# Optimization experiments

Measured on AMD Instinct MI355X. Metric: run time of the kernel, lower is better.

## Reference

```python
import jax, jax.numpy as jnp
import numpy as np

HEADS = 8
DIM_HEAD = 64

def setup_inputs() -> dict:
    key = jax.random.key(0)
    ks = jax.random.split(key, 5)
    B, N, D = 2, 4096, 512  # query_dim = inner_dim = 512
    s = 0.02
    return {
        "x": jax.random.normal(ks[0], (B, N, D), dtype=jnp.float32),
        "Wq": jax.random.normal(ks[1], (D, D), dtype=jnp.float32) * s,
        "Wk": jax.random.normal(ks[2], (D, D), dtype=jnp.float32) * s,
        "Wv": jax.random.normal(ks[3], (D, D), dtype=jnp.float32) * s,
        "Wo": jax.random.normal(ks[4], (D, D), dtype=jnp.float32) * s,
        "bo": jnp.zeros((D,), dtype=jnp.float32),
    }

def reference(x, Wq, Wk, Wv, Wo, bo):
    B, N, D = x.shape
    h, dh = HEADS, DIM_HEAD
    scale = dh ** (-0.5)
    # self-attention: context = x
    q = x @ Wq  # [B, N, h*dh]
    k = x @ Wk
    v = x @ Wv
    # b n (h d) -> b h n d
    q = q.reshape(B, N, h, dh).transpose(0, 2, 1, 3)
    k = k.reshape(B, N, h, dh).transpose(0, 2, 1, 3)
    v = v.reshape(B, N, h, dh).transpose(0, 2, 1, 3)
    sim = jnp.einsum('bhid,bhjd->bhij', q, k) * scale  # full [B,h,N,N] matrix
    attn = jax.nn.softmax(sim, axis=-1)
    out = jnp.einsum('bhij,bhjd->bhid', attn, v)
    out = out.transpose(0, 2, 1, 3).reshape(B, N, h * dh)
    return out @ Wo + bo
```

## Files before the change

kernel.cpp:

```cpp
#include <hip/hip_runtime.h>
#include <hip/hip_bf16.h>
#include <stddef.h>
#include <stdint.h>

typedef __bf16 bf16_t;
typedef bf16_t bf16x8 __attribute__((ext_vector_type(8)));
typedef bf16_t bf16x4 __attribute__((ext_vector_type(4)));
typedef bf16_t bf16x2 __attribute__((ext_vector_type(2)));
typedef float floatx4 __attribute__((ext_vector_type(4)));
typedef float floatx16 __attribute__((ext_vector_type(16)));
typedef int   intx4  __attribute__((ext_vector_type(4)));

#define SEQ    4096
#define DMODEL 512
#define NH     8
#define BATCH  2
#define QSCALE 0.18033688011112042f

__device__ __forceinline__ void ld_lds16(const void* g, void* l) {
  __builtin_amdgcn_global_load_lds(
      (const __attribute__((address_space(1))) unsigned int*)g,
      (__attribute__((address_space(3))) unsigned int*)l, 16, 0, 0);
}

__global__ __launch_bounds__(256) void prep_k(
    const float* __restrict__ x,
    const float* __restrict__ W0, const float* __restrict__ W1,
    const float* __restrict__ W2, const float* __restrict__ W3,
    bf16_t* __restrict__ Wt, bf16_t* __restrict__ xb)
{
  if (blockIdx.z == 4) {
    const floatx4* xf = (const floatx4*)x;
    bf16x4* xo = (bf16x4*)xb;
    int base = (blockIdx.y * 16 + blockIdx.x) * 4096 + threadIdx.x;
    #pragma unroll
    for (int i = 0; i < 16; i++) {
      floatx4 v = xf[base + i * 256];
      xo[base + i * 256] = bf16x4{(bf16_t)v.x, (bf16_t)v.y, (bf16_t)v.z, (bf16_t)v.w};
    }
    return;
  }
  __shared__ float Ws[32][33];
  const float* W = (blockIdx.z == 0) ? W0 : (blockIdx.z == 1) ? W1
                 : (blockIdx.z == 2) ? W2 : W3;
  bf16_t* out = Wt + (size_t)blockIdx.z * DMODEL * DMODEL;
  const int tx = threadIdx.x & 31, ty = threadIdx.x >> 5;
  const int k0 = blockIdx.y * 32, n0 = blockIdx.x * 32;
  #pragma unroll
  for (int i = 0; i < 4; i++) {
    int kk = ty + i * 8;
    Ws[kk][tx] = W[(size_t)(k0 + kk) * DMODEL + n0 + tx];
  }
  __syncthreads();
  #pragma unroll
  for (int i = 0; i < 4; i++) {
    int nn = ty + i * 8;
    out[(size_t)(n0 + nn) * DMODEL + k0 + tx] = (bf16_t)Ws[tx][nn];
  }
}

__global__ __launch_bounds__(256) void qkv_k(
    const bf16_t* __restrict__ xb, const bf16_t* __restrict__ Wt,
    bf16_t* __restrict__ Qw, bf16_t* __restrict__ Ksw, bf16_t* __restrict__ Vsw)
{
  __shared__ __align__(16) char smem[2 * 1792 * 16];
  const int tid  = threadIdx.x;
  const int wave = tid >> 6;
  const int lane = tid & 63;
  const int lh   = lane >> 4, lm = lane & 15;
  const int bm   = blockIdx.x * 128;
  const int bn   = blockIdx.y * 32;

  int offA[4], ldsA[4];
  #pragma unroll
  for (int i = 0; i < 4; i++) {
    int S = i * 256 + wave * 64 + lane;
    int r = S >> 3, cc = (S & 7) ^ (r & 7);
    offA[i] = (bm + r) * DMODEL + cc * 8;
    ldsA[i] = (i * 256 + wave * 64) * 16;
  }
  int offB[3], ldsB[3];
  #pragma unroll
  for (int j = 0; j < 3; j++) {
    int S = j * 256 + wave * 64 + lane;
    int m = S >> 8, s2 = S & 255;
    int n = s2 >> 3, cc = (s2 & 7) ^ (n & 7);
    offB[j] = m * DMODEL * DMODEL + (bn + n) * DMODEL + cc * 8;
    ldsB[j] = (1024 + j * 256 + wave * 64) * 16;
  }

  floatx4 acc[3][2][2];
  #pragma unroll
  for (int m = 0; m < 3; m++)
    #pragma unroll
    for (int rb = 0; rb < 2; rb++)
      #pragma unroll
      for (int nb = 0; nb < 2; nb++)
        acc[m][rb][nb] = floatx4{0.f, 0.f, 0.f, 0.f};

  auto issue = [&](int kt, int buf) {
    char* bp = smem + buf * 1792 * 16;
    #pragma unroll
    for (int i = 0; i < 4; i++) ld_lds16(xb + offA[i] + kt * 64, bp + ldsA[i]);
    #pragma unroll
    for (int j = 0; j < 3; j++) ld_lds16(Wt + offB[j] + kt * 64, bp + ldsB[j]);
  };

  issue(0, 0);
  for (int kt = 0; kt < 8; kt++) {
    __syncthreads();
    if (kt < 7) issue(kt + 1, (kt + 1) & 1);
    const char* bp = smem + (kt & 1) * 1792 * 16;
    #pragma unroll
    for (int ks = 0; ks < 2; ks++) {
      int cc = ks * 4 + lh;
      int rA = wave * 32 + lm;
      bf16x8 a0 = *(const bf16x8*)(bp + (rA * 8 + (cc ^ (rA & 7))) * 16);
      bf16x8 a1 = *(const bf16x8*)(bp + ((rA + 16) * 8 + (cc ^ (rA & 7))) * 16);
      #pragma unroll
      for (int m = 0; m < 3; m++) {
        #pragma unroll
        for (int nb = 0; nb < 2; nb++) {
          int n = nb * 16 + lm;
          bf16x8 b = *(const bf16x8*)(bp + (1024 + m * 256 + n * 8 + (cc ^ (n & 7))) * 16);
          acc[m][0][nb] = __builtin_amdgcn_mfma_f32_16x16x32_bf16(a0, b, acc[m][0][nb], 0, 0, 0);
          acc[m][1][nb] = __builtin_amdgcn_mfma_f32_16x16x32_bf16(a1, b, acc[m][1][nb], 0, 0, 0);
        }
      }
    }
  }

  const int h  = bn >> 6;
  const int dl = bn & 63;
  #pragma unroll
  for (int rb = 0; rb < 2; rb++)
    #pragma unroll
    for (int nb = 0; nb < 2; nb++)
      #pragma unroll
      for (int r = 0; r < 4; r++) {
        int row = bm + wave * 32 + rb * 16 + lh * 4 + r;
        Qw[(size_t)row * DMODEL + bn + nb * 16 + lm] = (bf16_t)(acc[0][rb][nb][r] * QSCALE);
      }
  #pragma unroll
  for (int rb = 0; rb < 2; rb++)
    #pragma unroll
    for (int nb = 0; nb < 2; nb++) {
      int d = dl + nb * 16 + lm;
      #pragma unroll
      for (int r = 0; r < 4; r++) {
        int row = bm + wave * 32 + rb * 16 + lh * 4 + r;
        int bb = row >> 12, tk = row & 4095;
        size_t off = ((size_t)(bb * NH + h) * 64 + (tk >> 6)) * 4096
                   + (size_t)(tk & 63) * 64
                   + ((((d >> 3) ^ (tk & 7)) << 3) | (d & 7));
        Ksw[off] = (bf16_t)acc[1][rb][nb][r];
      }
    }
  bf16_t (*Ts)[136] = (bf16_t(*)[136])smem;
  __syncthreads();
  #pragma unroll
  for (int rb = 0; rb < 2; rb++)
    #pragma unroll
    for (int nb = 0; nb < 2; nb++) {
      int dloc = nb * 16 + lm, tok0 = wave * 32 + rb * 16 + lh * 4;
      bf16x4 v = {(bf16_t)acc[2][rb][nb][0], (bf16_t)acc[2][rb][nb][1],
                  (bf16_t)acc[2][rb][nb][2], (bf16_t)acc[2][rb][nb][3]};
      *(bf16x4*)&Ts[dloc][tok0] = v;
    }
  __syncthreads();
  {
    const int bb = bm >> 12, tk0 = bm & 4095;
    const size_t hb = (size_t)(bb * NH + h) * 64;
    #pragma unroll
    for (int i = 0; i < 2; i++) {
      int idx = tid + i * 256;
      int dloc = idx >> 4, c8 = idx & 15;
      int d = dl + dloc;
      bf16x8 val = *(bf16x8*)&Ts[dloc][c8 * 8];
      size_t off = (hb + (tk0 >> 6) + (c8 >> 3)) * 4096
                 + (size_t)d * 64 + (((c8 & 7) ^ (d & 7)) << 3);
      *(bf16x8*)&Vsw[off] = val;
    }
  }
}

__global__ __launch_bounds__(256) void out_k(
    const bf16_t* __restrict__ A, const bf16_t* __restrict__ Wt,
    const float* __restrict__ bias, float* __restrict__ out)
{
  __shared__ __align__(16) char smem[2 * 1536 * 16];
  const int tid  = threadIdx.x;
  const int wave = tid >> 6;
  const int lane = tid & 63;
  const int lh   = lane >> 4, lm = lane & 15;
  const int bm   = blockIdx.x * 128;
  const int bn   = blockIdx.y * 64;

  int offA[4], ldsA[4];
  #pragma unroll
  for (int i = 0; i < 4; i++) {
    int S = i * 256 + wave * 64 + lane;
    int r = S >> 3, cc = (S & 7) ^ (r & 7);
    offA[i] = (bm + r) * DMODEL + cc * 8;
    ldsA[i] = (i * 256 + wave * 64) * 16;
  }
  int offB[2], ldsB[2];
  #pragma unroll
  for (int j = 0; j < 2; j++) {
    int S = j * 256 + wave * 64 + lane;
    int n = S >> 3, cc = (S & 7) ^ (n & 7);
    offB[j] = (bn + n) * DMODEL + cc * 8;
    ldsB[j] = (1024 + j * 256 + wave * 64) * 16;
  }

  floatx4 acc[2][4];
  #pragma unroll
  for (int rb = 0; rb < 2; rb++)
    #pragma unroll
    for (int nb = 0; nb < 4; nb++) acc[rb][nb] = floatx4{0.f, 0.f, 0.f, 0.f};

  auto issue = [&](int kt, int buf) {
    char* bp = smem + buf * 1536 * 16;
    #pragma unroll
    for (int i = 0; i < 4; i++) ld_lds16(A + offA[i] + kt * 64, bp + ldsA[i]);
    #pragma unroll
    for (int j = 0; j < 2; j++) ld_lds16(Wt + offB[j] + kt * 64, bp + ldsB[j]);
  };

  issue(0, 0);
  for (int kt = 0; kt < 8; kt++) {
    __syncthreads();
    if (kt < 7) issue(kt + 1, (kt + 1) & 1);
    const char* bp = smem + (kt & 1) * 1536 * 16;
    #pragma unroll
    for (int ks = 0; ks < 2; ks++) {
      int cc = ks * 4 + lh;
      int rA = wave * 32 + lm;
      bf16x8 a0 = *(const bf16x8*)(bp + (rA * 8 + (cc ^ (rA & 7))) * 16);
      bf16x8 a1 = *(const bf16x8*)(bp + ((rA + 16) * 8 + (cc ^ (rA & 7))) * 16);
      #pragma unroll
      for (int nb = 0; nb < 4; nb++) {
        int n = nb * 16 + lm;
        bf16x8 b = *(const bf16x8*)(bp + (1024 + n * 8 + (cc ^ (n & 7))) * 16);
        acc[0][nb] = __builtin_amdgcn_mfma_f32_16x16x32_bf16(a0, b, acc[0][nb], 0, 0, 0);
        acc[1][nb] = __builtin_amdgcn_mfma_f32_16x16x32_bf16(a1, b, acc[1][nb], 0, 0, 0);
      }
    }
  }

  #pragma unroll
  for (int rb = 0; rb < 2; rb++)
    #pragma unroll
    for (int nb = 0; nb < 4; nb++) {
      float bv = bias[bn + nb * 16 + lm];
      #pragma unroll
      for (int r = 0; r < 4; r++) {
        int row = bm + wave * 32 + rb * 16 + lh * 4 + r;
        out[(size_t)row * DMODEL + bn + nb * 16 + lm] = acc[rb][nb][r] + bv;
      }
    }
}

__global__ __launch_bounds__(256) void attn_k(
    const bf16_t* __restrict__ Qw, const bf16_t* __restrict__ Ksw,
    const bf16_t* __restrict__ Vsw, bf16_t* __restrict__ Ow)
{
  __shared__ __align__(16) char smem[2 * 1024 * 16];
  const int tid  = threadIdx.x;
  const int wave = tid >> 6;
  const int lane = tid & 63;
  const int hi   = lane >> 5;
  const int lo   = lane & 31;
  const int bh   = blockIdx.y, b = bh >> 3, h = bh & 7;
  const int q0   = blockIdx.x * 128;
  const size_t kvbase = (size_t)bh * 64 * 4096;

  const int qrow_g = b * SEQ + q0 + wave * 32 + lo;
  bf16x8 qreg[4];
  #pragma unroll
  for (int i = 0; i < 4; i++)
    qreg[i] = *(const bf16x8*)&Qw[(size_t)qrow_g * DMODEL + h * 64 + i * 16 + hi * 8];

  floatx16 accO[2];
  #pragma unroll
  for (int nb = 0; nb < 2; nb++)
    #pragma unroll
    for (int j = 0; j < 16; j++) accO[nb][j] = 0.f;
  float ls0 = 0.f, ls1 = 0.f, ls2 = 0.f, ls3 = 0.f;

  auto issue = [&](int t, int buf) {
    char* bp = smem + buf * 16384;
    const bf16_t* ksrc = Ksw + kvbase + (size_t)t * 4096;
    const bf16_t* vsrc = Vsw + kvbase + (size_t)t * 4096;
    #pragma unroll
    for (int j = 0; j < 2; j++) {
      int base = j * 256 + wave * 64;
      ld_lds16(ksrc + (base + lane) * 8, bp + base * 16);
      ld_lds16(vsrc + (base + lane) * 8, bp + 8192 + base * 16);
    }
  };

  issue(0, 0);
  for (int t = 0; t < SEQ / 64; t++) {
    __syncthreads();
    if (t < SEQ / 64 - 1) issue(t + 1, (t + 1) & 1);
    const bf16_t* Kb = (const bf16_t*)(smem + (t & 1) * 16384);
    const bf16_t* Vb = Kb + 4096;

    floatx16 accS[2];
    #pragma unroll
    for (int nb = 0; nb < 2; nb++)
      #pragma unroll
      for (int j = 0; j < 16; j++) accS[nb][j] = 0.f;
    #pragma unroll
    for (int kd = 0; kd < 4; kd++) {
      #pragma unroll
      for (int nb = 0; nb < 2; nb++) {
        int row = nb * 32 + lo;
        bf16x8 ak = *(const bf16x8*)&Kb[row * 64 + (((kd * 2 + hi) ^ (row & 7)) << 3)];
        accS[nb] = __builtin_amdgcn_mfma_f32_32x32x16_bf16(ak, qreg[kd], accS[nb], 0, 0, 0);
      }
    }

    #pragma unroll
    for (int nb = 0; nb < 2; nb++) {
      float p[16];
      #pragma unroll
      for (int r = 0; r < 16; r++) p[r] = __builtin_amdgcn_exp2f(accS[nb][r]);
      #pragma unroll
      for (int r = 0; r < 16; r += 4) {
        ls0 += p[r]; ls1 += p[r + 1]; ls2 += p[r + 2]; ls3 += p[r + 3];
      }
      int pk[8];
      #pragma unroll
      for (int i = 0; i < 8; i++) {
        bf16x2 t2 = {(bf16_t)p[2 * i], (bf16_t)p[2 * i + 1]};
        pk[i] = __builtin_bit_cast(int, t2);
      }
      #pragma unroll
      for (int c2 = 0; c2 < 2; c2++) {
        int s0 = hi ? pk[4 * c2 + 0] : pk[4 * c2 + 2];
        int s1 = hi ? pk[4 * c2 + 1] : pk[4 * c2 + 3];
        int r0 = __shfl_xor(s0, 32, 64);
        int r1 = __shfl_xor(s1, 32, 64);
        intx4 pi;
        pi.x = hi ? r0 : pk[4 * c2 + 0];
        pi.y = hi ? r1 : pk[4 * c2 + 1];
        pi.z = hi ? pk[4 * c2 + 2] : r0;
        pi.w = hi ? pk[4 * c2 + 3] : r1;
        bf16x8 pf = __builtin_bit_cast(bf16x8, pi);
        int c = nb * 2 + c2;
        #pragma unroll
        for (int nbo = 0; nbo < 2; nbo++) {
          int row = nbo * 32 + lo;
          bf16x8 av = *(const bf16x8*)&Vb[row * 64 + (((c * 2 + hi) ^ (row & 7)) << 3)];
          accO[nbo] = __builtin_amdgcn_mfma_f32_32x32x16_bf16(av, pf, accO[nbo], 0, 0, 0);
        }
      }
    }
  }

  float lsum = (ls0 + ls1) + (ls2 + ls3);
  lsum += __shfl_xor(lsum, 32, 64);
  float linv = 1.0f / lsum;

  __syncthreads();
  bf16_t* Os = (bf16_t*)smem + wave * 2048;
  #pragma unroll
  for (int nb = 0; nb < 2; nb++)
    #pragma unroll
    for (int g = 0; g < 4; g++) {
      int dbase = g * 8 + 4 * hi + 32 * nb;
      bf16x4 v4 = {(bf16_t)(accO[nb][4 * g + 0] * linv),
                   (bf16_t)(accO[nb][4 * g + 1] * linv),
                   (bf16_t)(accO[nb][4 * g + 2] * linv),
                   (bf16_t)(accO[nb][4 * g + 3] * linv)};
      *(bf16x4*)&Os[lo * 64 + (dbase ^ ((lo & 7) << 3))] = v4;
    }
  #pragma unroll
  for (int i = 0; i < 4; i++) {
    int chunk = i * 64 + lane;
    int q = chunk >> 3, c8 = chunk & 7;
    bf16x8 v = *(const bf16x8*)&Os[q * 64 + ((c8 ^ (q & 7)) << 3)];
    int row_g = b * SEQ + q0 + wave * 32 + q;
    *(bf16x8*)&Ow[(size_t)row_g * DMODEL + h * 64 + c8 * 8] = v;
  }
}

extern "C" void kernel_launch(void* const* d_in, const int* in_sizes, int n_in,
                              void* d_out, int out_size, void* d_ws, size_t ws_size,
                              hipStream_t stream)
{
  const float* x  = (const float*)d_in[0];
  const float* Wq = (const float*)d_in[1];
  const float* Wk = (const float*)d_in[2];
  const float* Wv = (const float*)d_in[3];
  const float* Wo = (const float*)d_in[4];
  const float* bo = (const float*)d_in[5];
  float* out = (float*)d_out;

  const int M = BATCH * SEQ;
  const size_t WT = (size_t)DMODEL * DMODEL;
  const size_t E  = (size_t)M * DMODEL;
  if (ws_size < (4 * WT + 3 * E) * sizeof(bf16_t)) return;

  bf16_t* Wt  = (bf16_t*)d_ws;
  bf16_t* Qw  = Wt + 4 * WT;
  bf16_t* Ksw = Qw + E;
  bf16_t* Vsw = Ksw + E;
  bf16_t* Ow  = Qw;
  bf16_t* xbf = (bf16_t*)d_out;

  prep_k<<<dim3(16, 16, 5), 256, 0, stream>>>(x, Wq, Wk, Wv, Wo, Wt, xbf);

  qkv_k<<<dim3(M / 128, DMODEL / 32), 256, 0, stream>>>(xbf, Wt, Qw, Ksw, Vsw);

  attn_k<<<dim3(SEQ / 128, BATCH * NH), 256, 0, stream>>>(Qw, Ksw, Vsw, Ow);

  out_k<<<dim3(M / 128, DMODEL / 64), 256, 0, stream>>>(Ow, Wt + 3 * WT, bo, out);
}
```

Measured before the change: 184.9 us.

## Split attention KV across wave pairs and retile QKV projection per mode/head

The attention kernel now gives each wave 64 query rows and half of a 128-key tile, with the two halves of each key tile handled by different wave pairs. Partial outputs and row sums are merged through shared memory at the end. This reuses each K/V fragment across two query chunks and halves the number of loop iterations, at the cost of a larger LDS footprint and extra accumulator registers, with launch bounds set to 2 blocks per CU. The QKV projection now uses one grid slice per (Q/K/V, head) with 64-wide output tiles and a rewritten V transpose store. The softmax also drops the cross-lane shuffle for P and instead relies on a different key ordering.

```diff
diff --git a/kernel.cpp b/kernel.cpp
--- a/kernel.cpp
+++ b/kernel.cpp
@@ -63,13 +63,16 @@
     const bf16_t* __restrict__ xb, const bf16_t* __restrict__ Wt,
     bf16_t* __restrict__ Qw, bf16_t* __restrict__ Ksw, bf16_t* __restrict__ Vsw)
 {
-  __shared__ __align__(16) char smem[2 * 1792 * 16];
+  __shared__ __align__(16) char smem[2 * 1536 * 16];
   const int tid  = threadIdx.x;
   const int wave = tid >> 6;
   const int lane = tid & 63;
   const int lh   = lane >> 4, lm = lane & 15;
   const int bm   = blockIdx.x * 128;
-  const int bn   = blockIdx.y * 32;
+  const int mode = blockIdx.y >> 3;
+  const int h    = blockIdx.y & 7;
+  const bf16_t* Wm = Wt + (size_t)mode * DMODEL * DMODEL;
+  const int bn   = h * 64;
 
   int offA[4], ldsA[4];
   #pragma unroll
@@ -79,38 +82,34 @@
     offA[i] = (bm + r) * DMODEL + cc * 8;
     ldsA[i] = (i * 256 + wave * 64) * 16;
   }
-  int offB[3], ldsB[3];
-  #pragma unroll
-  for (int j = 0; j < 3; j++) {
+  int offB[2], ldsB[2];
+  #pragma unroll
+  for (int j = 0; j < 2; j++) {
     int S = j * 256 + wave * 64 + lane;
-    int m = S >> 8, s2 = S & 255;
-    int n = s2 >> 3, cc = (s2 & 7) ^ (n & 7);
-    offB[j] = m * DMODEL * DMODEL + (bn + n) * DMODEL + cc * 8;
+    int n = S >> 3, cc = (S & 7) ^ (n & 7);
+    offB[j] = (bn + n) * DMODEL + cc * 8;
     ldsB[j] = (1024 + j * 256 + wave * 64) * 16;
   }
 
-  floatx4 acc[3][2][2];
-  #pragma unroll
-  for (int m = 0; m < 3; m++)
-    #pragma unroll
-    for (int rb = 0; rb < 2; rb++)
-      #pragma unroll
-      for (int nb = 0; nb < 2; nb++)
-        acc[m][rb][nb] = floatx4{0.f, 0.f, 0.f, 0.f};
+  floatx4 acc[2][4];
+  #pragma unroll
+  for (int rb = 0; rb < 2; rb++)
+    #pragma unroll
+    for (int nb = 0; nb < 4; nb++) acc[rb][nb] = floatx4{0.f, 0.f, 0.f, 0.f};
 
   auto issue = [&](int kt, int buf) {
-    char* bp = smem + buf * 1792 * 16;
+    char* bp = smem + buf * 1536 * 16;
     #pragma unroll
     for (int i = 0; i < 4; i++) ld_lds16(xb + offA[i] + kt * 64, bp + ldsA[i]);
     #pragma unroll
-    for (int j = 0; j < 3; j++) ld_lds16(Wt + offB[j] + kt * 64, bp + ldsB[j]);
+    for (int j = 0; j < 2; j++) ld_lds16(Wm + offB[j] + kt * 64, bp + ldsB[j]);
   };
 
   issue(0, 0);
   for (int kt = 0; kt < 8; kt++) {
     __syncthreads();
     if (kt < 7) issue(kt + 1, (kt + 1) & 1);
-    const char* bp = smem + (kt & 1) * 1792 * 16;
+    const char* bp = smem + (kt & 1) * 1536 * 16;
     #pragma unroll
     for (int ks = 0; ks < 2; ks++) {
       int cc = ks * 4 + lh;
@@ -118,68 +117,69 @@
       bf16x8 a0 = *(const bf16x8*)(bp + (rA * 8 + (cc ^ (rA & 7))) * 16);
       bf16x8 a1 = *(const bf16x8*)(bp + ((rA + 16) * 8 + (cc ^ (rA & 7))) * 16);
       #pragma unroll
-      for (int m = 0; m < 3; m++) {
-        #pragma unroll
-        for (int nb = 0; nb < 2; nb++) {
-          int n = nb * 16 + lm;
-          bf16x8 b = *(const bf16x8*)(bp + (1024 + m * 256 + n * 8 + (cc ^ (n & 7))) * 16);
-          acc[m][0][nb] = __builtin_amdgcn_mfma_f32_16x16x32_bf16(a0, b, acc[m][0][nb], 0, 0, 0);
-          acc[m][1][nb] = __builtin_amdgcn_mfma_f32_16x16x32_bf16(a1, b, acc[m][1][nb], 0, 0, 0);
-        }
-      }
-    }
-  }
-
-  const int h  = bn >> 6;
-  const int dl = bn & 63;
-  #pragma unroll
-  for (int rb = 0; rb < 2; rb++)
-    #pragma unroll
-    for (int nb = 0; nb < 2; nb++)
-      #pragma unroll
-      for (int r = 0; r < 4; r++) {
-        int row = bm + wave * 32 + rb * 16 + lh * 4 + r;
-        Qw[(size_t)row * DMODEL + bn + nb * 16 + lm] = (bf16_t)(acc[0][rb][nb][r] * QSCALE);
-      }
-  #pragma unroll
-  for (int rb = 0; rb < 2; rb++)
-    #pragma unroll
-    for (int nb = 0; nb < 2; nb++) {
-      int d = dl + nb * 16 + lm;
-      #pragma unroll
-      for (int r = 0; r < 4; r++) {
-        int row = bm + wave * 32 + rb * 16 + lh * 4 + r;
-        int bb = row >> 12, tk = row & 4095;
-        size_t off = ((size_t)(bb * NH + h) * 64 + (tk >> 6)) * 4096
-                   + (size_t)(tk & 63) * 64
-                   + ((((d >> 3) ^ (tk & 7)) << 3) | (d & 7));
-        Ksw[off] = (bf16_t)acc[1][rb][nb][r];
-      }
-    }
-  bf16_t (*Ts)[136] = (bf16_t(*)[136])smem;
-  __syncthreads();
-  #pragma unroll
-  for (int rb = 0; rb < 2; rb++)
-    #pragma unroll
-    for (int nb = 0; nb < 2; nb++) {
-      int dloc = nb * 16 + lm, tok0 = wave * 32 + rb * 16 + lh * 4;
-      bf16x4 v = {(bf16_t)acc[2][rb][nb][0], (bf16_t)acc[2][rb][nb][1],
-                  (bf16_t)acc[2][rb][nb][2], (bf16_t)acc[2][rb][nb][3]};
-      *(bf16x4*)&Ts[dloc][tok0] = v;
-    }
-  __syncthreads();
-  {
+      for (int nb = 0; nb < 4; nb++) {
+        int n = nb * 16 + lm;
+        bf16x8 b = *(const bf16x8*)(bp + (1024 + n * 8 + (cc ^ (n & 7))) * 16);
+        acc[0][nb] = __builtin_amdgcn_mfma_f32_16x16x32_bf16(a0, b, acc[0][nb], 0, 0, 0);
+        acc[1][nb] = __builtin_amdgcn_mfma_f32_16x16x32_bf16(a1, b, acc[1][nb], 0, 0, 0);
+      }
+    }
+  }
+
+  if (mode == 0) {
+    #pragma unroll
+    for (int rb = 0; rb < 2; rb++)
+      #pragma unroll
+      for (int nb = 0; nb < 4; nb++)
+        #pragma unroll
+        for (int r = 0; r < 4; r++) {
+          int row = bm + wave * 32 + rb * 16 + lh * 4 + r;
+          Qw[(size_t)row * DMODEL + bn + nb * 16 + lm] =
+              (bf16_t)(acc[rb][nb][r] * QSCALE);
+        }
+  } else if (mode == 1) {
+    #pragma unroll
+    for (int rb = 0; rb < 2; rb++)
+      #pragma unroll
+      for (int nb = 0; nb < 4; nb++) {
+        int d = nb * 16 + lm;
+        #pragma unroll
+        for (int r = 0; r < 4; r++) {
+          int row = bm + wave * 32 + rb * 16 + lh * 4 + r;
+          int bb = row >> 12, tk = row & 4095;
+          size_t off = ((size_t)(bb * NH + h) * 64 + (tk >> 6)) * 4096
+                     + (size_t)(tk & 63) * 64
+                     + ((((d >> 3) ^ (tk & 7)) << 3) | (d & 7));
+          Ksw[off] = (bf16_t)acc[rb][nb][r];
+        }
+      }
+  } else {
+    __syncthreads();
+    bf16_t (*Ts)[136] = (bf16_t(*)[136])smem;
+    #pragma unroll
+    for (int rb = 0; rb < 2; rb++)
+      #pragma unroll
+      for (int nb = 0; nb < 4; nb++) {
+        int dloc = nb * 16 + lm, tok0 = wave * 32 + rb * 16 + lh * 4;
+        bf16x4 v = {(bf16_t)acc[rb][nb][0], (bf16_t)acc[rb][nb][1],
+                    (bf16_t)acc[rb][nb][2], (bf16_t)acc[rb][nb][3]};
+        *(bf16x4*)&Ts[dloc][tok0] = v;
+      }
+    __syncthreads();
     const int bb = bm >> 12, tk0 = bm & 4095;
     const size_t hb = (size_t)(bb * NH + h) * 64;
     #pragma unroll
-    for (int i = 0; i < 2; i++) {
+    for (int i = 0; i < 4; i++) {
       int idx = tid + i * 256;
-      int dloc = idx >> 4, c8 = idx & 15;
-      int d = dl + dloc;
-      bf16x8 val = *(bf16x8*)&Ts[dloc][c8 * 8];
-      size_t off = (hb + (tk0 >> 6) + (c8 >> 3)) * 4096
-                 + (size_t)d * 64 + (((c8 & 7) ^ (d & 7)) << 3);
-      *(bf16x8*)&Vsw[off] = val;
+      int d = idx >> 4, c8 = idx & 15;
+      bf16x8 val = *(bf16x8*)&Ts[d][c8 * 8];
+      int cw = c8 & 7;
+      int g = cw >> 1, sub = cw & 1;
+      size_t tbase = (hb + (tk0 >> 6) + (c8 >> 3)) * 4096 + (size_t)d * 64;
+      bf16x4 v0 = {val[0], val[1], val[2], val[3]};
+      bf16x4 v1 = {val[4], val[5], val[6], val[7]};
+      *(bf16x4*)&Vsw[tbase + (((2 * g) ^ (d & 7)) << 3) + sub * 4] = v0;
+      *(bf16x4*)&Vsw[tbase + (((2 * g + 1) ^ (d & 7)) << 3) + sub * 4] = v1;
     }
   }
 }
@@ -261,13 +261,14 @@
     }
 }
 
-__global__ __launch_bounds__(256) void attn_k(
+__global__ __launch_bounds__(256, 2) void attn_k(
     const bf16_t* __restrict__ Qw, const bf16_t* __restrict__ Ksw,
     const bf16_t* __restrict__ Vsw, bf16_t* __restrict__ Ow)
 {
-  __shared__ __align__(16) char smem[2 * 1024 * 16];
+  __shared__ __align__(16) char smem[2 * 32768];
   const int tid  = threadIdx.x;
   const int wave = tid >> 6;
+  const int qh   = wave & 1, kh = wave >> 1;
   const int lane = tid & 63;
   const int hi   = lane >> 5;
   const int lo   = lane & 31;
@@ -275,115 +276,166 @@
   const int q0   = blockIdx.x * 128;
   const size_t kvbase = (size_t)bh * 64 * 4096;
 
-  const int qrow_g = b * SEQ + q0 + wave * 32 + lo;
-  bf16x8 qreg[4];
-  #pragma unroll
-  for (int i = 0; i < 4; i++)
-    qreg[i] = *(const bf16x8*)&Qw[(size_t)qrow_g * DMODEL + h * 64 + i * 16 + hi * 8];
-
-  floatx16 accO[2];
-  #pragma unroll
-  for (int nb = 0; nb < 2; nb++)
-    #pragma unroll
-    for (int j = 0; j < 16; j++) accO[nb][j] = 0.f;
-  float ls0 = 0.f, ls1 = 0.f, ls2 = 0.f, ls3 = 0.f;
-
-  auto issue = [&](int t, int buf) {
-    char* bp = smem + buf * 16384;
-    const bf16_t* ksrc = Ksw + kvbase + (size_t)t * 4096;
-    const bf16_t* vsrc = Vsw + kvbase + (size_t)t * 4096;
+  bf16x8 qreg[2][4];
+  #pragma unroll
+  for (int qc = 0; qc < 2; qc++) {
+    int qrow_g = b * SEQ + q0 + qh * 64 + qc * 32 + lo;
+    #pragma unroll
+    for (int i = 0; i < 4; i++)
+      qreg[qc][i] = *(const bf16x8*)&Qw[(size_t)qrow_g * DMODEL + h * 64 + i * 16 + hi * 8];
+  }
+
+  floatx16 accO[2][2];
+  #pragma unroll
+  for (int qc = 0; qc < 2; qc++)
+    #pragma unroll
+    for (int nbo = 0; nbo < 2; nbo++)
+      #pragma unroll
+      for (int j = 0; j < 16; j++) accO[qc][nbo][j] = 0.f;
+  float ls[2] = {0.f, 0.f};
+
+  auto issue = [&](int s, int buf) {
+    char* bp = smem + buf * 32768;
     #pragma unroll
     for (int j = 0; j < 2; j++) {
-      int base = j * 256 + wave * 64;
-      ld_lds16(ksrc + (base + lane) * 8, bp + base * 16);
-      ld_lds16(vsrc + (base + lane) * 8, bp + 8192 + base * 16);
+      const bf16_t* ksrc = Ksw + kvbase + (size_t)(2 * s + j) * 4096;
+      const bf16_t* vsrc = Vsw + kvbase + (size_t)(2 * s + j) * 4096;
+      #pragma unroll
+      for (int half = 0; half < 2; half++) {
+        int base = half * 256 + wave * 64;
+        ld_lds16(ksrc + (base + lane) * 8, bp + j * 16384 + base * 16);
+        ld_lds16(vsrc + (base + lane) * 8, bp + j * 16384 + 8192 + base * 16);
+      }
     }
   };
 
   issue(0, 0);
-  for (int t = 0; t < SEQ / 64; t++) {
+  for (int s = 0; s < SEQ / 128; s++) {
     __syncthreads();
-    if (t < SEQ / 64 - 1) issue(t + 1, (t + 1) & 1);
-    const bf16_t* Kb = (const bf16_t*)(smem + (t & 1) * 16384);
+    if (s < SEQ / 128 - 1) issue(s + 1, (s + 1) & 1);
+    const bf16_t* Kb = (const bf16_t*)(smem + (s & 1) * 32768 + kh * 16384);
     const bf16_t* Vb = Kb + 4096;
 
-    floatx16 accS[2];
-    #pragma unroll
-    for (int nb = 0; nb < 2; nb++)
-      #pragma unroll
-      for (int j = 0; j < 16; j++) accS[nb][j] = 0.f;
+    floatx16 accS[2][2];
+    #pragma unroll
+    for (int qc = 0; qc < 2; qc++)
+      #pragma unroll
+      for (int nb = 0; nb < 2; nb++)
+        #pragma unroll
+        for (int j = 0; j < 16; j++) accS[qc][nb][j] = 0.f;
     #pragma unroll
     for (int kd = 0; kd < 4; kd++) {
       #pragma unroll
       for (int nb = 0; nb < 2; nb++) {
         int row = nb * 32 + lo;
         bf16x8 ak = *(const bf16x8*)&Kb[row * 64 + (((kd * 2 + hi) ^ (row & 7)) << 3)];
-        accS[nb] = __builtin_amdgcn_mfma_f32_32x32x16_bf16(ak, qreg[kd], accS[nb], 0, 0, 0);
-      }
-    }
-
-    #pragma unroll
-    for (int nb = 0; nb < 2; nb++) {
-      float p[16];
-      #pragma unroll
-      for (int r = 0; r < 16; r++) p[r] = __builtin_amdgcn_exp2f(accS[nb][r]);
-      #pragma unroll
-      for (int r = 0; r < 16; r += 4) {
-        ls0 += p[r]; ls1 += p[r + 1]; ls2 += p[r + 2]; ls3 += p[r + 3];
-      }
-      int pk[8];
-      #pragma unroll
-      for (int i = 0; i < 8; i++) {
-        bf16x2 t2 = {(bf16_t)p[2 * i], (bf16_t)p[2 * i + 1]};
-        pk[i] = __builtin_bit_cast(int, t2);
-      }
-      #pragma unroll
-      for (int c2 = 0; c2 < 2; c2++) {
-        int s0 = hi ? pk[4 * c2 + 0] : pk[4 * c2 + 2];
-        int s1 = hi ? pk[4 * c2 + 1] : pk[4 * c2 + 3];
-        int r0 = __shfl_xor(s0, 32, 64);
-        int r1 = __shfl_xor(s1, 32, 64);
-        intx4 pi;
-        pi.x = hi ? r0 : pk[4 * c2 + 0];
-        pi.y = hi ? r1 : pk[4 * c2 + 1];
-        pi.z = hi ? pk[4 * c2 + 2] : r0;
-        pi.w = hi ? pk[4 * c2 + 3] : r1;
-        bf16x8 pf = __builtin_bit_cast(bf16x8, pi);
-        int c = nb * 2 + c2;
-        #pragma unroll
-        for (int nbo = 0; nbo < 2; nbo++) {
-          int row = nbo * 32 + lo;
-          bf16x8 av = *(const bf16x8*)&Vb[row * 64 + (((c * 2 + hi) ^ (row & 7)) << 3)];
-          accO[nbo] = __builtin_amdgcn_mfma_f32_32x32x16_bf16(av, pf, accO[nbo], 0, 0, 0);
-        }
-      }
-    }
-  }
-
-  float lsum = (ls0 + ls1) + (ls2 + ls3);
-  lsum += __shfl_xor(lsum, 32, 64);
-  float linv = 1.0f / lsum;
-
+        #pragma unroll
+        for (int qc = 0; qc < 2; qc++)
+          accS[qc][nb] = __builtin_amdgcn_mfma_f32_32x32x16_bf16(ak, qreg[qc][kd], accS[qc][nb], 0, 0, 0);
+      }
+    }
+
+    int pkq[2][2][8];
+    #pragma unroll
+    for (int qc = 0; qc < 2; qc++)
+      #pragma unroll
+      for (int nb = 0; nb < 2; nb++) {
+        float p[16];
+        #pragma unroll
+        for (int r = 0; r < 16; r++) p[r] = __builtin_amdgcn_exp2f(accS[qc][nb][r]);
+        #pragma unroll
+        for (int r = 0; r < 16; r += 4)
+          ls[qc] += (p[r] + p[r + 1]) + (p[r + 2] + p[r + 3]);
+        #pragma unroll
+        for (int i = 0; i < 8; i++) {
+          bf16x2 t2 = {(bf16_t)p[2 * i], (bf16_t)p[2 * i + 1]};
+          pkq[qc][nb][i] = __builtin_bit_cast(int, t2);
+        }
+      }
+
+    #pragma unroll
+    for (int c = 0; c < 4; c++) {
+      int nb = c >> 1, c2 = c & 1;
+      #pragma unroll
+      for (int nbo = 0; nbo < 2; nbo++) {
+        int row = nbo * 32 + lo;
+        bf16x8 av = *(const bf16x8*)&Vb[row * 64 + (((c * 2 + hi) ^ (row & 7)) << 3)];
+        #pragma unroll
+        for (int qc = 0; qc < 2; qc++) {
+          intx4 pi = {pkq[qc][nb][4 * c2], pkq[qc][nb][4 * c2 + 1],
+                      pkq[qc][nb][4 * c2 + 2], pkq[qc][nb][4 * c2 + 3]};
+          bf16x8 pf = __builtin_bit_cast(bf16x8, pi);
+          accO[qc][nbo] = __builtin_amdgcn_mfma_f32_32x32x16_bf16(av, pf, accO[qc][nbo], 0, 0, 0);
+        }
+      }
+    }
+  }
+
+  ls[0] += __shfl_xor(ls[0], 32, 64);
+  ls[1] += __shfl_xor(ls[1], 32, 64);
   __syncthreads();
-  bf16_t* Os = (bf16_t*)smem + wave * 2048;
-  #pragma unroll
-  for (int nb = 0; nb < 2; nb++)
-    #pragma unroll
-    for (int g = 0; g < 4; g++) {
-      int dbase = g * 8 + 4 * hi + 32 * nb;
-      bf16x4 v4 = {(bf16_t)(accO[nb][4 * g + 0] * linv),
-                   (bf16_t)(accO[nb][4 * g + 1] * linv),
-                   (bf16_t)(accO[nb][4 * g + 2] * linv),
-                   (bf16_t)(accO[nb][4 * g + 3] * linv)};
-      *(bf16x4*)&Os[lo * 64 + (dbase ^ ((lo & 7) << 3))] = v4;
-    }
-  #pragma unroll
-  for (int i = 0; i < 4; i++) {
-    int chunk = i * 64 + lane;
-    int q = chunk >> 3, c8 = chunk & 7;
-    bf16x8 v = *(const bf16x8*)&Os[q * 64 + ((c8 ^ (q & 7)) << 3)];
-    int row_g = b * SEQ + q0 + wave * 32 + q;
-    *(bf16x8*)&Ow[(size_t)row_g * DMODEL + h * 64 + c8 * 8] = v;
+  float* mrg = (float*)smem;
+  if (kh == 1) {
+    #pragma unroll
+    for (int qc = 0; qc < 2; qc++)
+      #pragma unroll
+      for (int nbo = 0; nbo < 2; nbo++) {
+        float* dst = mrg + qh * 4096 + (qc * 2 + nbo) * 1024 + lane * 16;
+        #pragma unroll
+        for (int g = 0; g < 4; g++) {
+          floatx4 v = {accO[qc][nbo][4 * g], accO[qc][nbo][4 * g + 1],
+                       accO[qc][nbo][4 * g + 2], accO[qc][nbo][4 * g + 3]};
+          *(floatx4*)(dst + 4 * g) = v;
+        }
+      }
+    if (hi == 0) {
+      mrg[8192 + qh * 128 + 0 * 64 + lo] = ls[0];
+      mrg[8192 + qh * 128 + 1 * 64 + lo] = ls[1];
+    }
+  }
+  __syncthreads();
+  if (kh == 0) {
+    float linv[2];
+    #pragma unroll
+    for (int qc = 0; qc < 2; qc++)
+      linv[qc] = 1.0f / (ls[qc] + mrg[8192 + qh * 128 + qc * 64 + lo]);
+    #pragma unroll
+    for (int qc = 0; qc < 2; qc++)
+      #pragma unroll
+      for (int nbo = 0; nbo < 2; nbo++) {
+        const float* src = mrg + qh * 4096 + (qc * 2 + nbo) * 1024 + lane * 16;
+        #pragma unroll
+        for (int g = 0; g < 4; g++) {
+          floatx4 v = *(const floatx4*)(src + 4 * g);
+          accO[qc][nbo][4 * g]     += v.x;
+          accO[qc][nbo][4 * g + 1] += v.y;
+          accO[qc][nbo][4 * g + 2] += v.z;
+          accO[qc][nbo][4 * g + 3] += v.w;
+        }
+      }
+    bf16_t* Os = (bf16_t*)(smem + 36864 + qh * 8192);
+    #pragma unroll
+    for (int qc = 0; qc < 2; qc++)
+      #pragma unroll
+      for (int nbo = 0; nbo < 2; nbo++)
+        #pragma unroll
+        for (int g = 0; g < 4; g++) {
+          int dbase = g * 8 + 4 * hi + 32 * nbo;
+          int qloc = qc * 32 + lo;
+          bf16x4 v4 = {(bf16_t)(accO[qc][nbo][4 * g] * linv[qc]),
+                       (bf16_t)(accO[qc][nbo][4 * g + 1] * linv[qc]),
+                       (bf16_t)(accO[qc][nbo][4 * g + 2] * linv[qc]),
+                       (bf16_t)(accO[qc][nbo][4 * g + 3] * linv[qc])};
+          *(bf16x4*)&Os[qloc * 64 + (dbase ^ ((qloc & 7) << 3))] = v4;
+        }
+    #pragma unroll
+    for (int i = 0; i < 8; i++) {
+      int idx = i * 64 + lane;
+      int q = idx >> 3, c8 = idx & 7;
+      bf16x8 v = *(const bf16x8*)&Os[q * 64 + ((c8 ^ (q & 7)) << 3)];
+      int row_g = b * SEQ + q0 + qh * 64 + q;
+      *(bf16x8*)&Ow[(size_t)row_g * DMODEL + h * 64 + c8 * 8] = v;
+    }
   }
 }
 
@@ -413,7 +465,7 @@
 
   prep_k<<<dim3(16, 16, 5), 256, 0, stream>>>(x, Wq, Wk, Wv, Wo, Wt, xbf);
 
-  qkv_k<<<dim3(M / 128, DMODEL / 32), 256, 0, stream>>>(xbf, Wt, Qw, Ksw, Vsw);
+  qkv_k<<<dim3(M / 128, 24), 256, 0, stream>>>(xbf, Wt, Qw, Ksw, Vsw);
 
   attn_k<<<dim3(SEQ / 128, BATCH * NH), 256, 0, stream>>>(Qw, Ksw, Vsw, Ow);
 
```

Measured after the change: 177.6 us. -4.0%, faster.

## Split attention KV loop across two wave groups and reorder V layout to drop shuffles

Applied to the files above, without the earlier changes.

The attention kernel now runs 512 threads: each query tile is handled by two waves that process alternate 64-key blocks of each 128-key stage, then merge partial outputs and row sums through LDS. The V scatter in the QKV kernel writes a permuted layout so the P fragments can be fed to the PV MFMA directly, which removes the cross-half shuffles. The aim is more waves in flight and less per-iteration overhead. The cost is a larger LDS footprint, an extra merge step at the end, and more register pressure under the new launch bounds.

```diff
diff --git a/kernel.cpp b/kernel.cpp
--- a/kernel.cpp
+++ b/kernel.cpp
@@ -177,9 +177,13 @@
       int dloc = idx >> 4, c8 = idx & 15;
       int d = dl + dloc;
       bf16x8 val = *(bf16x8*)&Ts[dloc][c8 * 8];
-      size_t off = (hb + (tk0 >> 6) + (c8 >> 3)) * 4096
-                 + (size_t)d * 64 + (((c8 & 7) ^ (d & 7)) << 3);
-      *(bf16x8*)&Vsw[off] = val;
+      int cw = c8 & 7;
+      int g = cw >> 1, sub = cw & 1;
+      size_t tbase = (hb + (tk0 >> 6) + (c8 >> 3)) * 4096 + (size_t)d * 64;
+      bf16x4 v0 = {val[0], val[1], val[2], val[3]};
+      bf16x4 v1 = {val[4], val[5], val[6], val[7]};
+      *(bf16x4*)&Vsw[tbase + (((2 * g) ^ (d & 7)) << 3) + sub * 4] = v0;
+      *(bf16x4*)&Vsw[tbase + (((2 * g + 1) ^ (d & 7)) << 3) + sub * 4] = v1;
     }
   }
 }
@@ -261,13 +265,15 @@
     }
 }
 
-__global__ __launch_bounds__(256) void attn_k(
+__global__ __launch_bounds__(512, 4) void attn_k(
     const bf16_t* __restrict__ Qw, const bf16_t* __restrict__ Ksw,
     const bf16_t* __restrict__ Vsw, bf16_t* __restrict__ Ow)
 {
-  __shared__ __align__(16) char smem[2 * 1024 * 16];
+  __shared__ __align__(16) char smem[2 * 32768];
   const int tid  = threadIdx.x;
   const int wave = tid >> 6;
+  const int qh   = wave >> 1;
+  const int kh   = wave & 1;
   const int lane = tid & 63;
   const int hi   = lane >> 5;
   const int lo   = lane & 31;
@@ -275,7 +281,7 @@
   const int q0   = blockIdx.x * 128;
   const size_t kvbase = (size_t)bh * 64 * 4096;
 
-  const int qrow_g = b * SEQ + q0 + wave * 32 + lo;
+  const int qrow_g = b * SEQ + q0 + qh * 32 + lo;
   bf16x8 qreg[4];
   #pragma unroll
   for (int i = 0; i < 4; i++)
@@ -283,28 +289,26 @@
 
   floatx16 accO[2];
   #pragma unroll
-  for (int nb = 0; nb < 2; nb++)
-    #pragma unroll
-    for (int j = 0; j < 16; j++) accO[nb][j] = 0.f;
-  float ls0 = 0.f, ls1 = 0.f, ls2 = 0.f, ls3 = 0.f;
-
-  auto issue = [&](int t, int buf) {
-    char* bp = smem + buf * 16384;
-    const bf16_t* ksrc = Ksw + kvbase + (size_t)t * 4096;
-    const bf16_t* vsrc = Vsw + kvbase + (size_t)t * 4096;
-    #pragma unroll
-    for (int j = 0; j < 2; j++) {
-      int base = j * 256 + wave * 64;
-      ld_lds16(ksrc + (base + lane) * 8, bp + base * 16);
-      ld_lds16(vsrc + (base + lane) * 8, bp + 8192 + base * 16);
-    }
+  for (int nbo = 0; nbo < 2; nbo++)
+    #pragma unroll
+    for (int j = 0; j < 16; j++) accO[nbo][j] = 0.f;
+  float ls = 0.f;
+
+  auto issue = [&](int s, int buf) {
+    char* bp = smem + buf * 32768;
+    const bf16_t* k0 = Ksw + kvbase + (size_t)(2 * s) * 4096;
+    const bf16_t* v0 = Vsw + kvbase + (size_t)(2 * s) * 4096;
+    ld_lds16(k0 + tid * 8,        bp + tid * 16);
+    ld_lds16(v0 + tid * 8,        bp + 8192 + tid * 16);
+    ld_lds16(k0 + 4096 + tid * 8, bp + 16384 + tid * 16);
+    ld_lds16(v0 + 4096 + tid * 8, bp + 24576 + tid * 16);
   };
 
   issue(0, 0);
-  for (int t = 0; t < SEQ / 64; t++) {
+  for (int s = 0; s < SEQ / 128; s++) {
     __syncthreads();
-    if (t < SEQ / 64 - 1) issue(t + 1, (t + 1) & 1);
-    const bf16_t* Kb = (const bf16_t*)(smem + (t & 1) * 16384);
+    if (s < SEQ / 128 - 1) issue(s + 1, (s + 1) & 1);
+    const bf16_t* Kb = (const bf16_t*)(smem + (s & 1) * 32768 + kh * 16384);
     const bf16_t* Vb = Kb + 4096;
 
     floatx16 accS[2];
@@ -322,68 +326,87 @@
       }
     }
 
+    int pk[2][8];
     #pragma unroll
     for (int nb = 0; nb < 2; nb++) {
       float p[16];
       #pragma unroll
       for (int r = 0; r < 16; r++) p[r] = __builtin_amdgcn_exp2f(accS[nb][r]);
       #pragma unroll
-      for (int r = 0; r < 16; r += 4) {
-        ls0 += p[r]; ls1 += p[r + 1]; ls2 += p[r + 2]; ls3 += p[r + 3];
-      }
-      int pk[8];
+      for (int r = 0; r < 16; r += 4)
+        ls += (p[r] + p[r + 1]) + (p[r + 2] + p[r + 3]);
       #pragma unroll
       for (int i = 0; i < 8; i++) {
         bf16x2 t2 = {(bf16_t)p[2 * i], (bf16_t)p[2 * i + 1]};
-        pk[i] = __builtin_bit_cast(int, t2);
-      }
-      #pragma unroll
-      for (int c2 = 0; c2 < 2; c2++) {
-        int s0 = hi ? pk[4 * c2 + 0] : pk[4 * c2 + 2];
-        int s1 = hi ? pk[4 * c2 + 1] : pk[4 * c2 + 3];
-        int r0 = __shfl_xor(s0, 32, 64);
-        int r1 = __shfl_xor(s1, 32, 64);
-        intx4 pi;
-        pi.x = hi ? r0 : pk[4 * c2 + 0];
-        pi.y = hi ? r1 : pk[4 * c2 + 1];
-        pi.z = hi ? pk[4 * c2 + 2] : r0;
-        pi.w = hi ? pk[4 * c2 + 3] : r1;
-        bf16x8 pf = __builtin_bit_cast(bf16x8, pi);
-        int c = nb * 2 + c2;
-        #pragma unroll
-        for (int nbo = 0; nbo < 2; nbo++) {
-          int row = nbo * 32 + lo;
-          bf16x8 av = *(const bf16x8*)&Vb[row * 64 + (((c * 2 + hi) ^ (row & 7)) << 3)];
-          accO[nbo] = __builtin_amdgcn_mfma_f32_32x32x16_bf16(av, pf, accO[nbo], 0, 0, 0);
-        }
-      }
-    }
-  }
-
-  float lsum = (ls0 + ls1) + (ls2 + ls3);
-  lsum += __shfl_xor(lsum, 32, 64);
-  float linv = 1.0f / lsum;
-
+        pk[nb][i] = __builtin_bit_cast(int, t2);
+      }
+    }
+
+    #pragma unroll
+    for (int c = 0; c < 4; c++) {
+      intx4 pi = {pk[c >> 1][4 * (c & 1)],     pk[c >> 1][4 * (c & 1) + 1],
+                  pk[c >> 1][4 * (c & 1) + 2], pk[c >> 1][4 * (c & 1) + 3]};
+      bf16x8 pf = __builtin_bit_cast(bf16x8, pi);
+      #pragma unroll
+      for (int nbo = 0; nbo < 2; nbo++) {
+        int row = nbo * 32 + lo;
+        bf16x8 av = *(const bf16x8*)&Vb[row * 64 + (((c * 2 + hi) ^ (row & 7)) << 3)];
+        accO[nbo] = __builtin_amdgcn_mfma_f32_32x32x16_bf16(av, pf, accO[nbo], 0, 0, 0);
+      }
+    }
+  }
+
+  ls += __shfl_xor(ls, 32, 64);
   __syncthreads();
-  bf16_t* Os = (bf16_t*)smem + wave * 2048;
-  #pragma unroll
-  for (int nb = 0; nb < 2; nb++)
-    #pragma unroll
-    for (int g = 0; g < 4; g++) {
-      int dbase = g * 8 + 4 * hi + 32 * nb;
-      bf16x4 v4 = {(bf16_t)(accO[nb][4 * g + 0] * linv),
-                   (bf16_t)(accO[nb][4 * g + 1] * linv),
-                   (bf16_t)(accO[nb][4 * g + 2] * linv),
-                   (bf16_t)(accO[nb][4 * g + 3] * linv)};
-      *(bf16x4*)&Os[lo * 64 + (dbase ^ ((lo & 7) << 3))] = v4;
-    }
-  #pragma unroll
-  for (int i = 0; i < 4; i++) {
-    int chunk = i * 64 + lane;
-    int q = chunk >> 3, c8 = chunk & 7;
-    bf16x8 v = *(const bf16x8*)&Os[q * 64 + ((c8 ^ (q & 7)) << 3)];
-    int row_g = b * SEQ + q0 + wave * 32 + q;
-    *(bf16x8*)&Ow[(size_t)row_g * DMODEL + h * 64 + c8 * 8] = v;
+  float* mrg = (float*)smem;
+  if (kh == 1) {
+    #pragma unroll
+    for (int nbo = 0; nbo < 2; nbo++) {
+      float* dst = mrg + qh * 2720 + nbo * 1360 + lane * 20;
+      #pragma unroll
+      for (int g = 0; g < 4; g++) {
+        dst[4 * g + 0] = accO[nbo][4 * g + 0];
+        dst[4 * g + 1] = accO[nbo][4 * g + 1];
+        dst[4 * g + 2] = accO[nbo][4 * g + 2];
+        dst[4 * g + 3] = accO[nbo][4 * g + 3];
+      }
+    }
+    if (hi == 0) mrg[10816 + qh * 32 + lo] = ls;
+  }
+  __syncthreads();
+  if (kh == 0) {
+    float linv = 1.0f / (ls + mrg[10816 + qh * 32 + lo]);
+    #pragma unroll
+    for (int nbo = 0; nbo < 2; nbo++) {
+      const float* src = mrg + qh * 2720 + nbo * 1360 + lane * 20;
+      #pragma unroll
+      for (int g = 0; g < 4; g++) {
+        accO[nbo][4 * g + 0] += src[4 * g + 0];
+        accO[nbo][4 * g + 1] += src[4 * g + 1];
+        accO[nbo][4 * g + 2] += src[4 * g + 2];
+        accO[nbo][4 * g + 3] += src[4 * g + 3];
+      }
+    }
+    bf16_t* Os = (bf16_t*)(smem + 49152 + qh * 4096);
+    #pragma unroll
+    for (int nbo = 0; nbo < 2; nbo++)
+      #pragma unroll
+      for (int g = 0; g < 4; g++) {
+        int dbase = g * 8 + 4 * hi + 32 * nbo;
+        bf16x4 v4 = {(bf16_t)(accO[nbo][4 * g] * linv),
+                     (bf16_t)(accO[nbo][4 * g + 1] * linv),
+                     (bf16_t)(accO[nbo][4 * g + 2] * linv),
+                     (bf16_t)(accO[nbo][4 * g + 3] * linv)};
+        *(bf16x4*)&Os[lo * 64 + (dbase ^ ((lo & 7) << 3))] = v4;
+      }
+    #pragma unroll
+    for (int i = 0; i < 4; i++) {
+      int idx = i * 64 + lane;
+      int q = idx >> 3, c8 = idx & 7;
+      bf16x8 v = *(const bf16x8*)&Os[q * 64 + ((c8 ^ (q & 7)) << 3)];
+      int row_g = b * SEQ + q0 + qh * 32 + q;
+      *(bf16x8*)&Ow[(size_t)row_g * DMODEL + h * 64 + c8 * 8] = v;
+    }
   }
 }
 
@@ -415,7 +438,7 @@
 
   qkv_k<<<dim3(M / 128, DMODEL / 32), 256, 0, stream>>>(xbf, Wt, Qw, Ksw, Vsw);
 
-  attn_k<<<dim3(SEQ / 128, BATCH * NH), 256, 0, stream>>>(Qw, Ksw, Vsw, Ow);
+  attn_k<<<dim3(SEQ / 128, BATCH * NH), 512, 0, stream>>>(Qw, Ksw, Vsw, Ow);
 
   out_k<<<dim3(M / 128, DMODEL / 64), 256, 0, stream>>>(Ow, Wt + 3 * WT, bo, out);
 }
```

New measurement: 172.3 us. 1.07x faster.
